# Kernel optimization log

Hardware: AMD Instinct MI355X
Metric: run time of the kernel (lower is better)

## Reference

```python
import jax, jax.numpy as jnp
import numpy as np

B, T, F, H = 4, 2048, 1024, 16
DK = F // H


def setup_inputs() -> dict:
    key = jax.random.key(0)
    ks = jax.random.split(key, 11)
    s = float(np.sqrt(1.0 / F))
    u = lambda k, shape: jax.random.uniform(k, shape, jnp.float32, -s, s)
    return {
        "query": jax.random.normal(ks[0], (B, T, F), jnp.float32),
        "key": jax.random.normal(ks[1], (B, T, F), jnp.float32),
        "value": jax.random.normal(ks[2], (B, T, F), jnp.float32),
        "mask": jnp.ones((B, 1, T), dtype=bool),
        "Wq": u(ks[3], (F, F)), "bq": u(ks[4], (F,)),
        "Wk": u(ks[5], (F, F)), "bk": u(ks[6], (F,)),
        "Wv": u(ks[7], (F, F)), "bv": u(ks[8], (F,)),
        "Wo": u(ks[9], (F, F)),
    }


def reference(query, key, value, mask, Wq, bq, Wk, bk, Wv, bv, Wo):
    b, t1, f = query.shape
    # project and split heads: (B, H, T, DK)
    q = (query @ Wq + bq).reshape(b, -1, H, DK).transpose(0, 2, 1, 3)
    k = (key @ Wk + bk).reshape(b, -1, H, DK).transpose(0, 2, 1, 3)
    v = (value @ Wv + bv).reshape(b, -1, H, DK).transpose(0, 2, 1, 3)
    # scaled dot-product scores (B, H, T1, T2)
    scores = jnp.einsum("bhqd,bhkd->bhqk", q, k) / jnp.sqrt(jnp.float32(DK))
    m = mask[:, None]  # (B, 1, 1|T1, T2)
    scores = jnp.where(m, scores, jnp.finfo(scores.dtype).min)
    attn = jax.nn.softmax(scores, axis=-1)
    attn = jnp.where(m, attn, 0.0)
    x = jnp.einsum("bhqk,bhkd->bhqd", attn, v)
    x = x.transpose(0, 2, 1, 3).reshape(b, t1, H * DK)
    return x @ Wo
```

## Files before the change

### kernel.cpp

```cpp
#include <hip/hip_runtime.h>
#include <hip/hip_bf16.h>
#include <math.h>

#define B_  4
#define T_  2048
#define F_  1024
#define H_  16

typedef short short4v __attribute__((ext_vector_type(4)));
typedef short short8  __attribute__((ext_vector_type(8)));
typedef float f32x4   __attribute__((ext_vector_type(4)));
typedef float f32x16  __attribute__((ext_vector_type(16)));

__device__ __forceinline__ short f2bf(float f) {
  __hip_bfloat16 h = __float2bfloat16(f);
  short s;
  __builtin_memcpy(&s, &h, 2);
  return s;
}

__device__ __forceinline__ unsigned cvt_pk_bf16(float lo, float hi) {
  unsigned r;
  asm("v_cvt_pk_bf16_f32 %0, %1, %2" : "=v"(r) : "v"(lo), "v"(hi));
  return r;
}

__device__ __forceinline__ void gload_lds16(const void* g, void* l) {
  __builtin_amdgcn_global_load_lds(
      (const __attribute__((address_space(1))) void*)g,
      (__attribute__((address_space(3))) void*)l, 16, 0, 0);
}

__device__ __forceinline__ void barrier_lgkm() {
  asm volatile("s_waitcnt lgkmcnt(0)" ::: "memory");
  __builtin_amdgcn_sched_barrier(0);
  __builtin_amdgcn_s_barrier();
}

__global__ __launch_bounds__(256) void k_cvt3_bf16(const float* __restrict__ q,
                                                   const float* __restrict__ k,
                                                   const float* __restrict__ v,
                                                   short* __restrict__ qo,
                                                   short* __restrict__ ko,
                                                   short* __restrict__ vo) {
  const int seg = blockIdx.x >> 12;
  const float* in  = seg == 0 ? q  : (seg == 1 ? k  : v);
  short*       out = seg == 0 ? qo : (seg == 1 ? ko : vo);
  size_t i = (((size_t)(blockIdx.x & 4095)) * 256 + threadIdx.x) * 8;
  float4 a = *(const float4*)(in + i);
  float4 b = *(const float4*)(in + i + 4);
  short8 o;
  o[0] = f2bf(a.x); o[1] = f2bf(a.y); o[2] = f2bf(a.z); o[3] = f2bf(a.w);
  o[4] = f2bf(b.x); o[5] = f2bf(b.y); o[6] = f2bf(b.z); o[7] = f2bf(b.w);
  *(short8*)(out + i) = o;
}

__global__ __launch_bounds__(256) void k_transpose4(const float* __restrict__ W0,
                                                    const float* __restrict__ W1,
                                                    const float* __restrict__ W2,
                                                    const float* __restrict__ W3,
                                                    short* __restrict__ T0,
                                                    short* __restrict__ T1,
                                                    short* __restrict__ T2,
                                                    short* __restrict__ T3) {
  __shared__ float t[64][65];
  const int z = blockIdx.z;
  const float* W = z == 0 ? W0 : (z == 1 ? W1 : (z == 2 ? W2 : W3));
  short*      Wt = z == 0 ? T0 : (z == 1 ? T1 : (z == 2 ? T2 : T3));
  const int x  = threadIdx.x & 63;
  const int y0 = threadIdx.x >> 6;
  const int n0 = blockIdx.x * 64;
  const int k0 = blockIdx.y * 64;
#pragma unroll
  for (int i = 0; i < 16; ++i) {
    int r = y0 * 16 + i;
    t[r][x] = W[(size_t)(k0 + r) * F_ + n0 + x];
  }
  __syncthreads();
#pragma unroll
  for (int i = 0; i < 16; ++i) {
    int r = y0 * 16 + i;
    Wt[(size_t)(n0 + r) * F_ + k0 + x] = f2bf(t[x][r]);
  }
}

template<int HAS_BIAS, int OUT_MODE>
__device__ __forceinline__ void gemm_body(short* __restrict__ aLds,
                                          short* __restrict__ bLds,
                                          const short* __restrict__ A,
                                          const short* __restrict__ Bt,
                                          const float* __restrict__ bias,
                                          void* __restrict__ Cout, int p, float oscale) {
  const int K = F_, N = F_;
  const int tid = threadIdx.x;
  const int w = tid >> 6, l = tid & 63;
  const int lr = l & 15, lg = l >> 4;
  const int L = (p & 7) * 64 + (p >> 3);
  const int rowBase = (L >> 3) * 128;
  const int colBase = (L & 7) * 128;
  const int wrow = (w >> 1) * 64, wcol = (w & 1) * 64;
  f32x4 acc[4][4] = {};

  int soff[4];
#pragma unroll
  for (int pp = 0; pp < 4; ++pp) {
    int s = tid + pp * 256;
    int srow = s >> 3;
    soff[pp] = srow * K + (((s & 7) ^ (srow & 7)) * 8);
  }
  const short* Abase = A  + (size_t)rowBase * K;
  const short* Bbase = Bt + (size_t)colBase * K;

  auto STAGE = [&](int bufi, int kt) {
#pragma unroll
    for (int pp = 0; pp < 4; ++pp)
      gload_lds16(Abase + soff[pp] + kt, (char*)(aLds + bufi * 8192) + (tid + pp * 256) * 16);
#pragma unroll
    for (int pp = 0; pp < 4; ++pp)
      gload_lds16(Bbase + soff[pp] + kt, (char*)(bLds + bufi * 8192) + (tid + pp * 256) * 16);
  };

  auto COMPUTE = [&](int buf) {
    const char* aB = (const char*)(aLds + buf * 8192);
    const char* bB = (const char*)(bLds + buf * 8192);
#pragma unroll
    for (int kh = 0; kh < 2; ++kh) {
      short8 af[4], bf[4];
#pragma unroll
      for (int m = 0; m < 4; ++m) {
        int row = wrow + m * 16 + lr;
        af[m] = *(const short8*)(aB + row * 128 + (((kh * 4 + lg) ^ (row & 7)) * 16));
      }
#pragma unroll
      for (int n = 0; n < 4; ++n) {
        int row = wcol + n * 16 + lr;
        bf[n] = *(const short8*)(bB + row * 128 + (((kh * 4 + lg) ^ (row & 7)) * 16));
      }
#pragma unroll
      for (int m = 0; m < 4; ++m)
#pragma unroll
        for (int n = 0; n < 4; ++n)
          acc[m][n] = __builtin_amdgcn_mfma_f32_16x16x32_bf16(af[m], bf[n], acc[m][n], 0, 0, 0);
    }
  };

  STAGE(0, 0);
  int buf = 0;
  for (int kt = 0; kt < K; kt += 64) {
    if (kt + 64 < K) {
      STAGE(buf ^ 1, kt + 64);
      asm volatile("s_waitcnt vmcnt(8)" ::: "memory");
    } else {
      asm volatile("s_waitcnt vmcnt(0)" ::: "memory");
    }
    __builtin_amdgcn_sched_barrier(0);
    __builtin_amdgcn_s_barrier();
    __builtin_amdgcn_sched_barrier(0);
    COMPUTE(buf);
    __builtin_amdgcn_sched_barrier(0);
    __builtin_amdgcn_s_barrier();
    buf ^= 1;
  }

  float bv[4];
#pragma unroll
  for (int n = 0; n < 4; ++n)
    bv[n] = HAS_BIAS ? bias[colBase + wcol + n * 16 + lr] : 0.f;
#pragma unroll
  for (int m = 0; m < 4; ++m)
#pragma unroll
    for (int n = 0; n < 4; ++n) {
      int col = colBase + wcol + n * 16 + lr;
      int row0 = rowBase + wrow + m * 16 + lg * 4;
      if (OUT_MODE == 2) {
        short4v o;
#pragma unroll
        for (int r = 0; r < 4; ++r) o[r] = f2bf((acc[m][n][r] + bv[n]) * oscale);
        *(short4v*)&((short*)Cout)[((size_t)((row0 >> 11) * 1024 + col)) * 2048 +
                                   (row0 & 2047)] = o;
      } else {
#pragma unroll
        for (int r = 0; r < 4; ++r) {
          float v = (acc[m][n][r] + bv[n]) * oscale;
          if (OUT_MODE == 1) ((short*)Cout)[(size_t)(row0 + r) * N + col] = f2bf(v);
          else               ((float*)Cout)[(size_t)(row0 + r) * N + col] = v;
        }
      }
    }
}

__global__ __launch_bounds__(256) void k_gemm_qkv(const short* __restrict__ qb,
                                                  const short* __restrict__ kb,
                                                  const short* __restrict__ vb,
                                                  const short* __restrict__ WqT,
                                                  const short* __restrict__ WkT,
                                                  const short* __restrict__ WvT,
                                                  const float* __restrict__ bq,
                                                  const float* __restrict__ bk,
                                                  const float* __restrict__ bv,
                                                  short* __restrict__ Qp,
                                                  short* __restrict__ Kp,
                                                  short* __restrict__ Vt,
                                                  float qscale) {
  __shared__ short aLds[2][128 * 64];
  __shared__ short bLds[2][128 * 64];
  const int seg = blockIdx.x >> 9;
  const int p = blockIdx.x & 511;
  if (seg == 0)      gemm_body<1, 1>(&aLds[0][0], &bLds[0][0], qb, WqT, bq, Qp, p, qscale);
  else if (seg == 1) gemm_body<1, 1>(&aLds[0][0], &bLds[0][0], kb, WkT, bk, Kp, p, 1.0f);
  else               gemm_body<1, 2>(&aLds[0][0], &bLds[0][0], vb, WvT, bv, Vt, p, 1.0f);
}

__global__ __launch_bounds__(256) void k_gemm_out(const short* __restrict__ Xp,
                                                  const short* __restrict__ WoT,
                                                  float* __restrict__ out) {
  __shared__ short aLds[2][128 * 64];
  __shared__ short bLds[2][128 * 64];
  gemm_body<0, 0>(&aLds[0][0], &bLds[0][0], Xp, WoT, nullptr, out, blockIdx.x, 1.0f);
}

__global__ __launch_bounds__(256) void k_flash(const short* __restrict__ Qp,
                                               const short* __restrict__ Kp,
                                               const short* __restrict__ Vt,
                                               short* __restrict__ Xp) {
  __shared__ __align__(16) short kLds[2][64 * 64];
  __shared__ __align__(16) short vLds[2][64 * 64];
  const int tid = threadIdx.x, w = tid >> 6, l = tid & 63;
  const int lo = l & 31, hi = l >> 5;
  const int p = blockIdx.x;
  const int L = (p & 7) * 128 + (p >> 3);
  const int bh = L >> 4, qblk = L & 15;
  const int b = bh >> 4;
  const int hbase = (bh & 15) * 64;
  const int qw0 = b * T_ + qblk * 128 + w * 32;
  const int kvrow0 = b * T_;
  const short* Vb = Vt + (size_t)bh * 64 * T_;

  short8 aq[4];
#pragma unroll
  for (int ds = 0; ds < 4; ++ds)
    aq[ds] = *(const short8*)&Qp[(size_t)(qw0 + lo) * F_ + hbase + ds * 16 + hi * 8];

  short8 ones;
#pragma unroll
  for (int j = 0; j < 8; ++j) ones[j] = (short)0x3F80;

  const short* kSrc[2];
  const short* vSrc[2];
  int ldsOff[2];
#pragma unroll
  for (int i = 0; i < 2; ++i) {
    int s = (w * 2 + i) * 64 + l;
    int srow = s >> 3;
    int schunk = ((s & 7) ^ (srow & 7)) * 8;
    kSrc[i] = Kp + (size_t)(kvrow0 + srow) * F_ + hbase + schunk;
    vSrc[i] = Vb + (size_t)srow * T_ + schunk;
    ldsOff[i] = (w * 2 + i) * 1024 + l * 16;
  }

  short8 kA0, kA1, vA0, vA1;
  short8 kB0, kB1, vB0, vB1;
#define LOADSET(K0, K1, V0, V1)                                            \
  do {                                                                     \
    K0 = *(const short8*)kSrc[0]; K1 = *(const short8*)kSrc[1];            \
    V0 = *(const short8*)vSrc[0]; V1 = *(const short8*)vSrc[1];            \
    kSrc[0] += 64 * F_; kSrc[1] += 64 * F_; vSrc[0] += 64; vSrc[1] += 64;  \
  } while (0)
#define WRITESET(bufi, K0, K1, V0, V1)                                     \
  do {                                                                     \
    *(short8*)((char*)(&kLds[bufi][0]) + ldsOff[0]) = K0;                  \
    *(short8*)((char*)(&kLds[bufi][0]) + ldsOff[1]) = K1;                  \
    *(short8*)((char*)(&vLds[bufi][0]) + ldsOff[0]) = V0;                  \
    *(short8*)((char*)(&vLds[bufi][0]) + ldsOff[1]) = V1;                  \
  } while (0)

  f32x16 acc[2] = {};
  f32x16 acc_l = {};

  auto COMPUTE = [&](int bufi) {
    f32x16 s[2] = {};
    __builtin_amdgcn_s_setprio(1);
#pragma unroll
    for (int ds = 0; ds < 4; ++ds)
#pragma unroll
      for (int st = 0; st < 2; ++st) {
        int row = st * 32 + lo;
        short8 kf = *(const short8*)((char*)(&kLds[bufi][0]) + row * 128 +
                                     (((2 * ds + hi) ^ (row & 7)) * 16));
        s[st] = __builtin_amdgcn_mfma_f32_32x32x16_bf16(kf, aq[ds], s[st], 0, 0, 0);
      }
    __builtin_amdgcn_s_setprio(0);

#pragma unroll
    for (int st = 0; st < 2; ++st)
#pragma unroll
      for (int r = 0; r < 16; ++r)
        s[st][r] = __builtin_amdgcn_exp2f(s[st][r]);

    short8 pa[4];
#pragma unroll
    for (int st = 0; st < 2; ++st)
#pragma unroll
      for (int half = 0; half < 2; ++half) {
        const int g0 = 2 * half, g1 = 2 * half + 1;
        unsigned A0 = cvt_pk_bf16(s[st][4 * g0 + 0], s[st][4 * g0 + 1]);
        unsigned A1 = cvt_pk_bf16(s[st][4 * g0 + 2], s[st][4 * g0 + 3]);
        unsigned B0 = cvt_pk_bf16(s[st][4 * g1 + 0], s[st][4 * g1 + 1]);
        unsigned B1 = cvt_pk_bf16(s[st][4 * g1 + 2], s[st][4 * g1 + 3]);
        asm volatile("v_permlane32_swap_b32 %0, %1" : "+v"(A0), "+v"(B0));
        asm volatile("v_permlane32_swap_b32 %0, %1" : "+v"(A1), "+v"(B1));
        uint4 u4 = {A0, A1, B0, B1};
        pa[st * 2 + half] = *(short8*)&u4;
      }

    __builtin_amdgcn_s_setprio(1);
#pragma unroll
    for (int ks = 0; ks < 4; ++ks) {
#pragma unroll
      for (int dsub = 0; dsub < 2; ++dsub) {
        int row = dsub * 32 + lo;
        short8 vf = *(const short8*)((char*)(&vLds[bufi][0]) + row * 128 +
                                     (((2 * ks + hi) ^ (row & 7)) * 16));
        acc[dsub] = __builtin_amdgcn_mfma_f32_32x32x16_bf16(pa[ks], vf, acc[dsub], 0, 0, 0);
      }
      acc_l = __builtin_amdgcn_mfma_f32_32x32x16_bf16(pa[ks], ones, acc_l, 0, 0, 0);
    }
    __builtin_amdgcn_s_setprio(0);
  };

  LOADSET(kA0, kA1, vA0, vA1);
  LOADSET(kB0, kB1, vB0, vB1);
  WRITESET(0, kA0, kA1, vA0, vA1);
  barrier_lgkm();
  for (int t = 0; t < 32; t += 2) {
    if (t + 2 < 32) LOADSET(kA0, kA1, vA0, vA1);
    WRITESET(1, kB0, kB1, vB0, vB1);
    COMPUTE(0);
    barrier_lgkm();
    if (t + 3 < 32) LOADSET(kB0, kB1, vB0, vB1);
    if (t + 2 < 32) WRITESET(0, kA0, kA1, vA0, vA1);
    COMPUTE(1);
    barrier_lgkm();
  }
#undef LOADSET
#undef WRITESET

#pragma unroll
  for (int dsub = 0; dsub < 2; ++dsub)
#pragma unroll
    for (int r = 0; r < 16; ++r) {
      int qr = (r & 3) + 8 * (r >> 2) + 4 * hi;
      Xp[(size_t)(qw0 + qr) * F_ + hbase + dsub * 32 + lo] =
          f2bf(acc[dsub][r] / acc_l[r]);
    }
}

extern "C" void kernel_launch(void* const* d_in, const int* in_sizes, int n_in,
                              void* d_out, int out_size, void* d_ws, size_t ws_size,
                              hipStream_t stream) {
  const float* query = (const float*)d_in[0];
  const float* key   = (const float*)d_in[1];
  const float* value = (const float*)d_in[2];
  const float* Wq = (const float*)d_in[4];
  const float* bq = (const float*)d_in[5];
  const float* Wk = (const float*)d_in[6];
  const float* bk = (const float*)d_in[7];
  const float* Wv = (const float*)d_in[8];
  const float* bv = (const float*)d_in[9];
  const float* Wo = (const float*)d_in[10];
  float* out = (float*)d_out;

  const size_t MB = 1u << 20;
  char* ws = (char*)d_ws;
  short* qb  = (short*)(ws +   0 * MB);
  short* kb  = (short*)(ws +  16 * MB);
  short* vb  = (short*)(ws +  32 * MB);
  short* WqT = (short*)(ws +  48 * MB);
  short* WkT = (short*)(ws +  50 * MB);
  short* WvT = (short*)(ws +  52 * MB);
  short* WoT = (short*)(ws +  54 * MB);
  short* Qp  = (short*)(ws +  56 * MB);
  short* Kp  = (short*)(ws +  72 * MB);
  short* Vt  = (short*)(ws +  88 * MB);
  short* Xp  = qb;

  dim3 blk(256);
  k_cvt3_bf16<<<3 * 4096, blk, 0, stream>>>(query, key, value, qb, kb, vb);
  k_transpose4<<<dim3(16, 16, 4), blk, 0, stream>>>(Wq, Wk, Wv, Wo, WqT, WkT, WvT, WoT);
  const float qscale = 0.125f * 1.44269504f;
  k_gemm_qkv<<<3 * 512, blk, 0, stream>>>(qb, kb, vb, WqT, WkT, WvT,
                                          bq, bk, bv, Qp, Kp, Vt, qscale);
  k_flash<<<(T_ / 128) * B_ * H_, blk, 0, stream>>>(Qp, Kp, Vt, Xp);
  k_gemm_out<<<512, blk, 0, stream>>>(Xp, WoT, out);
}
```

Baseline: 213.5 us.

## Load K fragments directly to registers and stage V via global_load_lds in flash

The flash attention kernel stops staging K through LDS. Each wave now loads its K MFMA fragments straight from global memory into registers, prefetching the next tile after the QK MFMAs. V is copied into double-buffered LDS with direct global-to-LDS loads, ordered by vmcnt waits and one barrier per iteration, which removes the register round trip and the LDS writes. The two prep kernels, bf16 conversion and weight transpose, are merged into one launch to save a kernel launch. The cost is redundant global K reads across waves, since every wave loads the same K tile, plus tighter vmcnt accounting that must match the number of outstanding loads.

```diff
diff --git a/kernel.cpp b/kernel.cpp
--- a/kernel.cpp
+++ b/kernel.cpp
@@ -31,46 +31,42 @@
       (__attribute__((address_space(3))) void*)l, 16, 0, 0);
 }
 
-__device__ __forceinline__ void barrier_lgkm() {
-  asm volatile("s_waitcnt lgkmcnt(0)" ::: "memory");
-  __builtin_amdgcn_sched_barrier(0);
-  __builtin_amdgcn_s_barrier();
-}
-
-__global__ __launch_bounds__(256) void k_cvt3_bf16(const float* __restrict__ q,
-                                                   const float* __restrict__ k,
-                                                   const float* __restrict__ v,
-                                                   short* __restrict__ qo,
-                                                   short* __restrict__ ko,
-                                                   short* __restrict__ vo) {
-  const int seg = blockIdx.x >> 12;
-  const float* in  = seg == 0 ? q  : (seg == 1 ? k  : v);
-  short*       out = seg == 0 ? qo : (seg == 1 ? ko : vo);
-  size_t i = (((size_t)(blockIdx.x & 4095)) * 256 + threadIdx.x) * 8;
-  float4 a = *(const float4*)(in + i);
-  float4 b = *(const float4*)(in + i + 4);
-  short8 o;
-  o[0] = f2bf(a.x); o[1] = f2bf(a.y); o[2] = f2bf(a.z); o[3] = f2bf(a.w);
-  o[4] = f2bf(b.x); o[5] = f2bf(b.y); o[6] = f2bf(b.z); o[7] = f2bf(b.w);
-  *(short8*)(out + i) = o;
-}
-
-__global__ __launch_bounds__(256) void k_transpose4(const float* __restrict__ W0,
-                                                    const float* __restrict__ W1,
-                                                    const float* __restrict__ W2,
-                                                    const float* __restrict__ W3,
-                                                    short* __restrict__ T0,
-                                                    short* __restrict__ T1,
-                                                    short* __restrict__ T2,
-                                                    short* __restrict__ T3) {
+__global__ __launch_bounds__(256) void k_prep(const float* __restrict__ q,
+                                              const float* __restrict__ k,
+                                              const float* __restrict__ v,
+                                              short* __restrict__ qo,
+                                              short* __restrict__ ko,
+                                              short* __restrict__ vo,
+                                              const float* __restrict__ W0,
+                                              const float* __restrict__ W1,
+                                              const float* __restrict__ W2,
+                                              const float* __restrict__ W3,
+                                              short* __restrict__ T0,
+                                              short* __restrict__ T1,
+                                              short* __restrict__ T2,
+                                              short* __restrict__ T3) {
+  if (blockIdx.x < 12288) {
+    const int seg = blockIdx.x >> 12;
+    const float* in  = seg == 0 ? q  : (seg == 1 ? k  : v);
+    short*       out = seg == 0 ? qo : (seg == 1 ? ko : vo);
+    size_t i = (((size_t)(blockIdx.x & 4095)) * 256 + threadIdx.x) * 8;
+    float4 a = *(const float4*)(in + i);
+    float4 b = *(const float4*)(in + i + 4);
+    short8 o;
+    o[0] = f2bf(a.x); o[1] = f2bf(a.y); o[2] = f2bf(a.z); o[3] = f2bf(a.w);
+    o[4] = f2bf(b.x); o[5] = f2bf(b.y); o[6] = f2bf(b.z); o[7] = f2bf(b.w);
+    *(short8*)(out + i) = o;
+    return;
+  }
   __shared__ float t[64][65];
-  const int z = blockIdx.z;
+  const int tz = blockIdx.x - 12288;
+  const int z = tz >> 8, rem = tz & 255;
   const float* W = z == 0 ? W0 : (z == 1 ? W1 : (z == 2 ? W2 : W3));
   short*      Wt = z == 0 ? T0 : (z == 1 ? T1 : (z == 2 ? T2 : T3));
   const int x  = threadIdx.x & 63;
   const int y0 = threadIdx.x >> 6;
-  const int n0 = blockIdx.x * 64;
-  const int k0 = blockIdx.y * 64;
+  const int n0 = (rem & 15) * 64;
+  const int k0 = (rem >> 4) * 64;
 #pragma unroll
   for (int i = 0; i < 16; ++i) {
     int r = y0 * 16 + i;
@@ -223,7 +219,6 @@
                                                const short* __restrict__ Kp,
                                                const short* __restrict__ Vt,
                                                short* __restrict__ Xp) {
-  __shared__ __align__(16) short kLds[2][64 * 64];
   __shared__ __align__(16) short vLds[2][64 * 64];
   const int tid = threadIdx.x, w = tid >> 6, l = tid & 63;
   const int lo = l & 31, hi = l >> 5;
@@ -245,51 +240,61 @@
 #pragma unroll
   for (int j = 0; j < 8; ++j) ones[j] = (short)0x3F80;
 
-  const short* kSrc[2];
+  const short* bK0 = Kp + (size_t)(kvrow0 + lo) * F_ + hbase + hi * 8;
+  const short* bK1 = Kp + (size_t)(kvrow0 + 32 + lo) * F_ + hbase + hi * 8;
+
+  short8 kf0[4], kf1[4];
+  auto LOAD_K = [&]() {
+#pragma unroll
+    for (int ds = 0; ds < 4; ++ds) {
+      kf0[ds] = *(const short8*)(bK0 + ds * 16);
+      kf1[ds] = *(const short8*)(bK1 + ds * 16);
+    }
+    bK0 += 64 * F_;
+    bK1 += 64 * F_;
+  };
+
   const short* vSrc[2];
-  int ldsOff[2];
+  int vDst[2];
 #pragma unroll
   for (int i = 0; i < 2; ++i) {
     int s = (w * 2 + i) * 64 + l;
     int srow = s >> 3;
     int schunk = ((s & 7) ^ (srow & 7)) * 8;
-    kSrc[i] = Kp + (size_t)(kvrow0 + srow) * F_ + hbase + schunk;
     vSrc[i] = Vb + (size_t)srow * T_ + schunk;
-    ldsOff[i] = (w * 2 + i) * 1024 + l * 16;
-  }
-
-  short8 kA0, kA1, vA0, vA1;
-  short8 kB0, kB1, vB0, vB1;
-#define LOADSET(K0, K1, V0, V1)                                            \
-  do {                                                                     \
-    K0 = *(const short8*)kSrc[0]; K1 = *(const short8*)kSrc[1];            \
-    V0 = *(const short8*)vSrc[0]; V1 = *(const short8*)vSrc[1];            \
-    kSrc[0] += 64 * F_; kSrc[1] += 64 * F_; vSrc[0] += 64; vSrc[1] += 64;  \
-  } while (0)
-#define WRITESET(bufi, K0, K1, V0, V1)                                     \
-  do {                                                                     \
-    *(short8*)((char*)(&kLds[bufi][0]) + ldsOff[0]) = K0;                  \
-    *(short8*)((char*)(&kLds[bufi][0]) + ldsOff[1]) = K1;                  \
-    *(short8*)((char*)(&vLds[bufi][0]) + ldsOff[0]) = V0;                  \
-    *(short8*)((char*)(&vLds[bufi][0]) + ldsOff[1]) = V1;                  \
-  } while (0)
+    vDst[i] = (w * 2 + i) * 1024;
+  }
+  auto STAGE_V = [&](int bufi) {
+#pragma unroll
+    for (int i = 0; i < 2; ++i) {
+      gload_lds16(vSrc[i], (char*)(&vLds[bufi][0]) + vDst[i]);
+      vSrc[i] += 64;
+    }
+  };
 
   f32x16 acc[2] = {};
   f32x16 acc_l = {};
 
-  auto COMPUTE = [&](int bufi) {
+  STAGE_V(0);
+  LOAD_K();
+  asm volatile("s_waitcnt vmcnt(0)" ::: "memory");
+  __builtin_amdgcn_sched_barrier(0);
+  __builtin_amdgcn_s_barrier();
+
+  for (int t = 0; t < 32; ++t) {
+    const int buf = t & 1;
+    if (t + 1 < 32) STAGE_V(buf ^ 1);
+
     f32x16 s[2] = {};
     __builtin_amdgcn_s_setprio(1);
 #pragma unroll
-    for (int ds = 0; ds < 4; ++ds)
-#pragma unroll
-      for (int st = 0; st < 2; ++st) {
-        int row = st * 32 + lo;
-        short8 kf = *(const short8*)((char*)(&kLds[bufi][0]) + row * 128 +
-                                     (((2 * ds + hi) ^ (row & 7)) * 16));
-        s[st] = __builtin_amdgcn_mfma_f32_32x32x16_bf16(kf, aq[ds], s[st], 0, 0, 0);
-      }
+    for (int ds = 0; ds < 4; ++ds) {
+      s[0] = __builtin_amdgcn_mfma_f32_32x32x16_bf16(kf0[ds], aq[ds], s[0], 0, 0, 0);
+      s[1] = __builtin_amdgcn_mfma_f32_32x32x16_bf16(kf1[ds], aq[ds], s[1], 0, 0, 0);
+    }
     __builtin_amdgcn_s_setprio(0);
+
+    if (t + 1 < 32) LOAD_K();
 
 #pragma unroll
     for (int st = 0; st < 2; ++st)
@@ -319,31 +324,25 @@
 #pragma unroll
       for (int dsub = 0; dsub < 2; ++dsub) {
         int row = dsub * 32 + lo;
-        short8 vf = *(const short8*)((char*)(&vLds[bufi][0]) + row * 128 +
+        short8 vf = *(const short8*)((char*)(&vLds[buf][0]) + row * 128 +
                                      (((2 * ks + hi) ^ (row & 7)) * 16));
         acc[dsub] = __builtin_amdgcn_mfma_f32_32x32x16_bf16(pa[ks], vf, acc[dsub], 0, 0, 0);
       }
       acc_l = __builtin_amdgcn_mfma_f32_32x32x16_bf16(pa[ks], ones, acc_l, 0, 0, 0);
     }
     __builtin_amdgcn_s_setprio(0);
-  };
-
-  LOADSET(kA0, kA1, vA0, vA1);
-  LOADSET(kB0, kB1, vB0, vB1);
-  WRITESET(0, kA0, kA1, vA0, vA1);
-  barrier_lgkm();
-  for (int t = 0; t < 32; t += 2) {
-    if (t + 2 < 32) LOADSET(kA0, kA1, vA0, vA1);
-    WRITESET(1, kB0, kB1, vB0, vB1);
-    COMPUTE(0);
-    barrier_lgkm();
-    if (t + 3 < 32) LOADSET(kB0, kB1, vB0, vB1);
-    if (t + 2 < 32) WRITESET(0, kA0, kA1, vA0, vA1);
-    COMPUTE(1);
-    barrier_lgkm();
-  }
-#undef LOADSET
-#undef WRITESET
+
+    if (t + 1 < 32)
+      asm volatile("s_waitcnt vmcnt(8)" ::: "memory");
+    else
+      asm volatile("s_waitcnt vmcnt(0)" ::: "memory");
+    __builtin_amdgcn_sched_barrier(0);
+    __builtin_amdgcn_s_barrier();
+    if (t + 1 < 32) {
+      asm volatile("s_waitcnt vmcnt(0)" ::: "memory");
+      __builtin_amdgcn_sched_barrier(0);
+    }
+  }
 
 #pragma unroll
   for (int dsub = 0; dsub < 2; ++dsub)
@@ -385,8 +384,8 @@
   short* Xp  = qb;
 
   dim3 blk(256);
-  k_cvt3_bf16<<<3 * 4096, blk, 0, stream>>>(query, key, value, qb, kb, vb);
-  k_transpose4<<<dim3(16, 16, 4), blk, 0, stream>>>(Wq, Wk, Wv, Wo, WqT, WkT, WvT, WoT);
+  k_prep<<<12288 + 1024, blk, 0, stream>>>(query, key, value, qb, kb, vb,
+                                           Wq, Wk, Wv, Wo, WqT, WkT, WvT, WoT);
   const float qscale = 0.125f * 1.44269504f;
   k_gemm_qkv<<<3 * 512, blk, 0, stream>>>(qb, kb, vb, WqT, WkT, WvT,
                                           bq, bk, bv, Qp, Kp, Vt, qscale);
```

Result: slower. 259.3 us (+21.4%).
